# Kernel optimization log

Measured on AMD Instinct MI355X. Metric: run time of the kernel, lower is better.

## Reference

```python
import jax, jax.numpy as jnp
import numpy as np

SEQ, BATCH, EMBED = 2048, 4, 768
NUM_HEADS = 12
HEAD_DIM = EMBED // NUM_HEADS
SCALING = HEAD_DIM ** -0.5


def setup_inputs() -> dict:
    key = jax.random.key(0)
    ks = jax.random.split(key, 9)
    std = 0.02
    d = {"x": jax.random.normal(ks[0], (SEQ, BATCH, EMBED), dtype=jnp.float32)}
    for i, n in enumerate(["q", "k", "v", "out"]):
        d[f"W{n}"] = jax.random.normal(ks[1 + 2 * i], (EMBED, EMBED), dtype=jnp.float32) * std
        d[f"b{n}"] = jax.random.normal(ks[2 + 2 * i], (EMBED,), dtype=jnp.float32) * std
    return d


def reference(x, Wq, bq, Wk, bk, Wv, bv, Wout, bout):
    # x: [tgt_len, bsz, embed_dim] (fairseq seq-first layout per forward body)
    T, B, E = x.shape
    H, Dh = NUM_HEADS, HEAD_DIM

    q = (x @ Wq.T + bq) * SCALING          # [T, B, E]
    k = x @ Wk.T + bk
    v = x @ Wv.T + bv

    # view(T, B*H, Dh).transpose(0, 1) -> [B*H, T, Dh]
    q = q.reshape(T, B * H, Dh).transpose(1, 0, 2)
    k = k.reshape(T, B * H, Dh).transpose(1, 0, 2)
    v = v.reshape(T, B * H, Dh).transpose(1, 0, 2)

    # bmm: [B*H, T, T] attention scores (full O(T^2) matrix, as in the original)
    scores = jnp.einsum('bqd,bkd->bqk', q, k)
    # util_softmax with onnx_trace=True: softmax in float32, then cast back
    probs = jax.nn.softmax(scores.astype(jnp.float32), axis=-1).astype(scores.dtype)
    # dropout p=0.0 -> identity

    attn = jnp.einsum('bqk,bkd->bqd', probs, v)           # [B*H, T, Dh]
    attn = attn.transpose(1, 0, 2).reshape(T, B, E)       # [T, B, E]
    return attn @ Wout.T + bout
```

## Files before the change

kernel.cpp:

```cpp
#include <hip/hip_runtime.h>
#include <hip/hip_bf16.h>

#define SEQ 2048
#define BATCH 4
#define EMBED 768
#define NHEAD 12
#define HDIM 64
#define NROWS (SEQ*BATCH)
#define GH (BATCH*NHEAD)
#define KVBLK 64

typedef __bf16 bf16;
typedef __attribute__((ext_vector_type(4))) __bf16 bf16x4;
typedef __attribute__((ext_vector_type(8))) __bf16 bf16x8;
typedef __attribute__((ext_vector_type(4))) float f32x4;

#define LOG2E 1.44269504088896340736f

__global__ __launch_bounds__(256) void cvt_kernel(const float* __restrict__ in,
                                                  bf16* __restrict__ out, int n4) {
  int i = blockIdx.x * 256 + threadIdx.x;
  if (i >= n4) return;
  float4 v = reinterpret_cast<const float4*>(in)[i];
  bf16x4 o;
  o[0] = (bf16)v.x; o[1] = (bf16)v.y; o[2] = (bf16)v.z; o[3] = (bf16)v.w;
  reinterpret_cast<bf16x4*>(out)[i] = o;
}

__global__ __launch_bounds__(256) void cvt_w4(const float* __restrict__ Wq,
                                              const float* __restrict__ Wk,
                                              const float* __restrict__ Wv,
                                              const float* __restrict__ Wo,
                                              bf16* __restrict__ Wqkvb,
                                              bf16* __restrict__ Wob) {
  const int n4 = EMBED * EMBED / 4;
  int i = blockIdx.x * 256 + threadIdx.x;
  if (i >= n4) return;
  const float* src;
  bf16* dst;
  switch (blockIdx.y) {
    case 0: src = Wq; dst = Wqkvb; break;
    case 1: src = Wk; dst = Wqkvb + EMBED * EMBED; break;
    case 2: src = Wv; dst = Wqkvb + 2 * EMBED * EMBED; break;
    default: src = Wo; dst = Wob; break;
  }
  float4 v = reinterpret_cast<const float4*>(src)[i];
  bf16x4 o;
  o[0] = (bf16)v.x; o[1] = (bf16)v.y; o[2] = (bf16)v.z; o[3] = (bf16)v.w;
  reinterpret_cast<bf16x4*>(dst)[i] = o;
}

__global__ __launch_bounds__(256) void gemm_qkv(const bf16* __restrict__ A,
                                                const bf16* __restrict__ B,
                                                const float* __restrict__ bq,
                                                const float* __restrict__ bk,
                                                const float* __restrict__ bv,
                                                bf16* __restrict__ Qh,
                                                bf16* __restrict__ Kh,
                                                bf16* __restrict__ Vt) {
  constexpr int K = EMBED;
  __shared__ bf16 As[128 * 32];
  __shared__ bf16 Bs[128 * 32];
  const int tid = threadIdx.x;
  const int l = tid & 63;
  const int w = tid >> 6;
  const int row0 = blockIdx.x * 128;
  const int col0 = blockIdx.y * 128;
  const int wm = (w >> 1) * 64;
  const int wn = (w & 1) * 64;
  const int l15 = l & 15, l4 = l >> 4;

  f32x4 acc[4][4] = {};

  for (int k0 = 0; k0 < K; k0 += 32) {
#pragma unroll
    for (int i = 0; i < 2; ++i) {
      int c = tid + i * 256;
      int r = c >> 2, cc = c & 3;
      __builtin_amdgcn_global_load_lds(
          (const __attribute__((address_space(1))) void*)(A + (size_t)(row0 + r) * K + k0 + cc * 8),
          (__attribute__((address_space(3))) void*)(As + c * 8), 16, 0, 0);
    }
#pragma unroll
    for (int i = 0; i < 2; ++i) {
      int c = tid + i * 256;
      int r = c >> 2, cc = c & 3;
      __builtin_amdgcn_global_load_lds(
          (const __attribute__((address_space(1))) void*)(B + (size_t)(col0 + r) * K + k0 + cc * 8),
          (__attribute__((address_space(3))) void*)(Bs + c * 8), 16, 0, 0);
    }
    __syncthreads();

    bf16x8 af[4], bfr[4];
#pragma unroll
    for (int i = 0; i < 4; ++i)
      af[i] = *reinterpret_cast<const bf16x8*>(&As[(wm + i * 16 + l15) * 32 + l4 * 8]);
#pragma unroll
    for (int j = 0; j < 4; ++j)
      bfr[j] = *reinterpret_cast<const bf16x8*>(&Bs[(wn + j * 16 + l15) * 32 + l4 * 8]);
#pragma unroll
    for (int i = 0; i < 4; ++i)
#pragma unroll
      for (int j = 0; j < 4; ++j)
        acc[i][j] = __builtin_amdgcn_mfma_f32_16x16x32_bf16(af[i], bfr[j], acc[i][j], 0, 0, 0);
    __syncthreads();
  }

  const int sel = blockIdx.y / 6;
  const float* bias = sel == 0 ? bq : (sel == 1 ? bk : bv);
  const int colbase = col0 - sel * EMBED;
#pragma unroll
  for (int i = 0; i < 4; ++i) {
#pragma unroll
    for (int j = 0; j < 4; ++j) {
      int col = colbase + wn + j * 16 + l15;
      float bia = bias[col];
#pragma unroll
      for (int r = 0; r < 4; ++r) {
        int row = row0 + wm + i * 16 + l4 * 4 + r;
        float v = acc[i][j][r] + bia;
        int t = row >> 2, bb = row & 3;
        int hh = col >> 6, d = col & 63;
        int g = bb * NHEAD + hh;
        if (sel == 0)      Qh[((size_t)g * SEQ + t) * HDIM + d] = (bf16)(v * (0.125f * LOG2E));
        else if (sel == 1) Kh[((size_t)g * SEQ + t) * HDIM + d] = (bf16)v;
        else               Vt[((size_t)g * HDIM + d) * SEQ + t] = (bf16)v;
      }
    }
  }
}

__global__ __launch_bounds__(256) void gemm_out(const bf16* __restrict__ A,
                                                const bf16* __restrict__ B,
                                                const float* __restrict__ bias,
                                                float* __restrict__ outp) {
  constexpr int K = EMBED;
  __shared__ bf16 As[128 * 32];
  __shared__ bf16 Bs[128 * 32];
  const int tid = threadIdx.x;
  const int l = tid & 63;
  const int w = tid >> 6;
  const int row0 = blockIdx.x * 128;
  const int col0 = blockIdx.y * 128;
  const int wm = (w >> 1) * 64;
  const int wn = (w & 1) * 64;
  const int l15 = l & 15, l4 = l >> 4;

  f32x4 acc[4][4] = {};

  for (int k0 = 0; k0 < K; k0 += 32) {
#pragma unroll
    for (int i = 0; i < 2; ++i) {
      int c = tid + i * 256;
      int r = c >> 2, cc = c & 3;
      __builtin_amdgcn_global_load_lds(
          (const __attribute__((address_space(1))) void*)(A + (size_t)(row0 + r) * K + k0 + cc * 8),
          (__attribute__((address_space(3))) void*)(As + c * 8), 16, 0, 0);
    }
#pragma unroll
    for (int i = 0; i < 2; ++i) {
      int c = tid + i * 256;
      int r = c >> 2, cc = c & 3;
      __builtin_amdgcn_global_load_lds(
          (const __attribute__((address_space(1))) void*)(B + (size_t)(col0 + r) * K + k0 + cc * 8),
          (__attribute__((address_space(3))) void*)(Bs + c * 8), 16, 0, 0);
    }
    __syncthreads();

    bf16x8 af[4], bfr[4];
#pragma unroll
    for (int i = 0; i < 4; ++i)
      af[i] = *reinterpret_cast<const bf16x8*>(&As[(wm + i * 16 + l15) * 32 + l4 * 8]);
#pragma unroll
    for (int j = 0; j < 4; ++j)
      bfr[j] = *reinterpret_cast<const bf16x8*>(&Bs[(wn + j * 16 + l15) * 32 + l4 * 8]);
#pragma unroll
    for (int i = 0; i < 4; ++i)
#pragma unroll
      for (int j = 0; j < 4; ++j)
        acc[i][j] = __builtin_amdgcn_mfma_f32_16x16x32_bf16(af[i], bfr[j], acc[i][j], 0, 0, 0);
    __syncthreads();
  }

#pragma unroll
  for (int i = 0; i < 4; ++i) {
#pragma unroll
    for (int j = 0; j < 4; ++j) {
      int col = col0 + wn + j * 16 + l15;
      float bia = bias[col];
#pragma unroll
      for (int r = 0; r < 4; ++r) {
        int row = row0 + wm + i * 16 + l4 * 4 + r;
        outp[(size_t)row * EMBED + col] = acc[i][j][r] + bia;
      }
    }
  }
}

__global__ __launch_bounds__(256, 4) void attn_kernel(const bf16* __restrict__ Qh,
                                                      const bf16* __restrict__ Kh,
                                                      const bf16* __restrict__ Vt,
                                                      bf16* __restrict__ attnb) {
  const int g = blockIdx.x % GH;
  const int q0 = (blockIdx.x / GH) * 128;
  const int tid = threadIdx.x;
  const int w = tid >> 6, l = tid & 63;
  const int l15 = l & 15, l4 = l >> 4;
  const int qw = q0 + w * 32;

  __shared__ bf16 Ks[2][KVBLK * HDIM];
  __shared__ bf16 Vs[HDIM * KVBLK];
  __shared__ bf16 P_all[4][32 * 64];

  bf16* P = (bf16*)P_all[w];
  const bf16* Qp = Qh + (size_t)g * SEQ * HDIM;
  const bf16* Kp = Kh + (size_t)g * SEQ * HDIM;
  const bf16* Vp = Vt + (size_t)g * HDIM * SEQ;

#define STAGE_K(buf, kv0)                                                               \
  do {                                                                                  \
    _Pragma("unroll") for (int i = 0; i < 2; ++i) {                                     \
      int t = i * 256 + tid;                                                            \
      int r = t >> 3, c = t & 7;                                                        \
      __builtin_amdgcn_global_load_lds(                                                 \
          (const __attribute__((address_space(1))) void*)(Kp + (size_t)((kv0) + r) * HDIM + ((c ^ (r & 7)) * 8)), \
          (__attribute__((address_space(3))) void*)(&Ks[buf][t * 8]), 16, 0, 0);        \
    }                                                                                   \
  } while (0)

#define STAGE_V(kv0)                                                                    \
  do {                                                                                  \
    _Pragma("unroll") for (int i = 0; i < 2; ++i) {                                     \
      int t = i * 256 + tid;                                                            \
      int r = t >> 3, c = t & 7;                                                        \
      __builtin_amdgcn_global_load_lds(                                                 \
          (const __attribute__((address_space(1))) void*)(Vp + (size_t)r * SEQ + (kv0) + ((c ^ (r & 7)) * 8)), \
          (__attribute__((address_space(3))) void*)(&Vs[t * 8]), 16, 0, 0);             \
    }                                                                                   \
  } while (0)

  bf16x8 aq[2][2];
#pragma unroll
  for (int qf = 0; qf < 2; ++qf)
#pragma unroll
    for (int ks = 0; ks < 2; ++ks)
      aq[qf][ks] = *reinterpret_cast<const bf16x8*>(
          Qp + (size_t)(qw + qf * 16 + l15) * HDIM + ks * 32 + l4 * 8);

  bf16x8 vone;
#pragma unroll
  for (int i = 0; i < 8; ++i) vone[i] = (bf16)1.0f;

  f32x4 acco[2][4] = {};
  f32x4 accs[2] = {};

  STAGE_K(0, 0);
  __syncthreads();

  int cur = 0;
  for (int kv0 = 0; kv0 < SEQ; kv0 += KVBLK) {
    STAGE_V(kv0);
    STAGE_K(cur ^ 1, (kv0 + KVBLK) & (SEQ - 1));

    f32x4 s[2][4] = {};
#pragma unroll
    for (int kf = 0; kf < 4; ++kf) {
      int row = kf * 16 + l15;
#pragma unroll
      for (int ks = 0; ks < 2; ++ks) {
        bf16x8 bk = *reinterpret_cast<const bf16x8*>(
            &Ks[cur][row * 64 + (((ks * 4 + l4) ^ (row & 7)) * 8)]);
        __builtin_amdgcn_s_setprio(1);
        s[0][kf] = __builtin_amdgcn_mfma_f32_16x16x32_bf16(bk, aq[0][ks], s[0][kf], 0, 0, 0);
        s[1][kf] = __builtin_amdgcn_mfma_f32_16x16x32_bf16(bk, aq[1][ks], s[1][kf], 0, 0, 0);
        __builtin_amdgcn_s_setprio(0);
      }
    }

#pragma unroll
    for (int qf = 0; qf < 2; ++qf) {
      int prow = qf * 16 + l15;
#pragma unroll
      for (int kf = 0; kf < 4; ++kf) {
        float p0 = exp2f(s[qf][kf][0]);
        float p1 = exp2f(s[qf][kf][1]);
        float p2 = exp2f(s[qf][kf][2]);
        float p3 = exp2f(s[qf][kf][3]);
        bf16x4 pk;
        pk[0] = (bf16)p0; pk[1] = (bf16)p1; pk[2] = (bf16)p2; pk[3] = (bf16)p3;
        int chunk = (2 * kf + (l4 >> 1)) ^ (prow & 7);
        *reinterpret_cast<bf16x4*>(&P[prow * 64 + chunk * 8 + (l4 & 1) * 4]) = pk;
      }
    }

    asm volatile("s_waitcnt vmcnt(2)" ::: "memory");

#pragma unroll
    for (int ks = 0; ks < 2; ++ks) {
      bf16x8 ap[2];
#pragma unroll
      for (int qf = 0; qf < 2; ++qf) {
        int prow = qf * 16 + l15;
        int lc = ks * 4 + l4;
        ap[qf] = *reinterpret_cast<const bf16x8*>(P + prow * 64 + ((lc ^ (prow & 7)) << 3));
      }
#pragma unroll
      for (int df = 0; df < 4; ++df) {
        int row = df * 16 + l15;
        bf16x8 bv = *reinterpret_cast<const bf16x8*>(
            &Vs[row * 64 + (((ks * 4 + l4) ^ (row & 7)) * 8)]);
        __builtin_amdgcn_s_setprio(1);
        acco[0][df] = __builtin_amdgcn_mfma_f32_16x16x32_bf16(ap[0], bv, acco[0][df], 0, 0, 0);
        acco[1][df] = __builtin_amdgcn_mfma_f32_16x16x32_bf16(ap[1], bv, acco[1][df], 0, 0, 0);
        __builtin_amdgcn_s_setprio(0);
      }
      __builtin_amdgcn_s_setprio(1);
      accs[0] = __builtin_amdgcn_mfma_f32_16x16x32_bf16(ap[0], vone, accs[0], 0, 0, 0);
      accs[1] = __builtin_amdgcn_mfma_f32_16x16x32_bf16(ap[1], vone, accs[1], 0, 0, 0);
      __builtin_amdgcn_s_setprio(0);
    }
    __syncthreads();
    cur ^= 1;
  }

  const int bb = g / NHEAD, hh = g % NHEAD;
#pragma unroll
  for (int qf = 0; qf < 2; ++qf)
#pragma unroll
    for (int r = 0; r < 4; ++r) {
      float rinv = __builtin_amdgcn_rcpf(accs[qf][r]);
      int tq = qw + qf * 16 + l4 * 4 + r;
#pragma unroll
      for (int df = 0; df < 4; ++df) {
        int d = df * 16 + l15;
        attnb[((size_t)tq * BATCH + bb) * EMBED + hh * HDIM + d] = (bf16)(acco[qf][df][r] * rinv);
      }
    }
}

extern "C" void kernel_launch(void* const* d_in, const int* in_sizes, int n_in,
                              void* d_out, int out_size, void* d_ws, size_t ws_size,
                              hipStream_t stream) {
  const float* x  = (const float*)d_in[0];
  const float* Wq = (const float*)d_in[1];
  const float* bq = (const float*)d_in[2];
  const float* Wk = (const float*)d_in[3];
  const float* bk = (const float*)d_in[4];
  const float* Wv = (const float*)d_in[5];
  const float* bv = (const float*)d_in[6];
  const float* Wo = (const float*)d_in[7];
  const float* bo = (const float*)d_in[8];
  float* out = (float*)d_out;

  char* ws = (char*)d_ws;
  bf16* xb    = (bf16*)(ws + 0);
  bf16* Wqkvb = (bf16*)(ws + 12582912);
  bf16* Wob   = (bf16*)(ws + 16121856);
  bf16* Qh    = (bf16*)(ws + 17301504);
  bf16* Kh    = (bf16*)(ws + 29884416);
  bf16* Vt    = (bf16*)(ws + 42467328);
  bf16* attnb = (bf16*)(ws + 55050240);

  cvt_kernel<<<6144, 256, 0, stream>>>(x, xb, NROWS * EMBED / 4);
  cvt_w4<<<dim3(576, 4), 256, 0, stream>>>(Wq, Wk, Wv, Wo, Wqkvb, Wob);

  gemm_qkv<<<dim3(NROWS / 128, 18), 256, 0, stream>>>(xb, Wqkvb, bq, bk, bv, Qh, Kh, Vt);

  attn_kernel<<<GH * (SEQ / 128), 256, 0, stream>>>(Qh, Kh, Vt, attnb);

  gemm_out<<<dim3(NROWS / 128, EMBED / 128), 256, 0, stream>>>(attnb, Wob, bo, out);
}
```

Measured before the change: 168.3 us.

## Split attention KV range into two halves and combine partial outputs

Each attention workgroup now processes only half of the key/value sequence, doubling the grid from 768 to 1536 blocks to improve occupancy across compute units. Unnormalized partial outputs go to two bf16 buffers (reusing the xb workspace and attnb) along with per-row exp-sums. A new combine kernel adds the partials and normalizes. This works without rescaling because the kernel does not subtract a running max. It adds an extra pass over the attention output and rounds the unnormalized partials to bf16.

```diff
diff --git a/kernel.cpp b/kernel.cpp
--- a/kernel.cpp
+++ b/kernel.cpp
@@ -9,6 +9,7 @@
 #define NROWS (SEQ*BATCH)
 #define GH (BATCH*NHEAD)
 #define KVBLK 64
+#define KVHALF (SEQ/2)
 
 typedef __bf16 bf16;
 typedef __attribute__((ext_vector_type(4))) __bf16 bf16x4;
@@ -200,9 +201,14 @@
 __global__ __launch_bounds__(256, 4) void attn_kernel(const bf16* __restrict__ Qh,
                                                       const bf16* __restrict__ Kh,
                                                       const bf16* __restrict__ Vt,
-                                                      bf16* __restrict__ attnb) {
+                                                      bf16* __restrict__ O0,
+                                                      bf16* __restrict__ O1,
+                                                      float* __restrict__ Sums) {
   const int g = blockIdx.x % GH;
-  const int q0 = (blockIdx.x / GH) * 128;
+  const int r2 = blockIdx.x / GH;
+  const int half = r2 & 1;
+  const int q0 = (r2 >> 1) * 128;
+  const int kvbase = half * KVHALF;
   const int tid = threadIdx.x;
   const int w = tid >> 6, l = tid & 63;
   const int l15 = l & 15, l4 = l >> 4;
@@ -254,13 +260,13 @@
   f32x4 acco[2][4] = {};
   f32x4 accs[2] = {};
 
-  STAGE_K(0, 0);
+  STAGE_K(0, kvbase);
   __syncthreads();
 
   int cur = 0;
-  for (int kv0 = 0; kv0 < SEQ; kv0 += KVBLK) {
+  for (int kv0 = kvbase; kv0 < kvbase + KVHALF; kv0 += KVBLK) {
     STAGE_V(kv0);
-    STAGE_K(cur ^ 1, (kv0 + KVBLK) & (SEQ - 1));
+    STAGE_K(cur ^ 1, kvbase + (((kv0 - kvbase) + KVBLK) & (KVHALF - 1)));
 
     f32x4 s[2][4] = {};
 #pragma unroll
@@ -323,19 +329,43 @@
     cur ^= 1;
   }
 
+  bf16* Op = half ? O1 : O0;
+  float* Sp = Sums + (size_t)half * GH * SEQ + (size_t)g * SEQ;
   const int bb = g / NHEAD, hh = g % NHEAD;
 #pragma unroll
   for (int qf = 0; qf < 2; ++qf)
 #pragma unroll
     for (int r = 0; r < 4; ++r) {
-      float rinv = __builtin_amdgcn_rcpf(accs[qf][r]);
       int tq = qw + qf * 16 + l4 * 4 + r;
+      if (l15 == 0) Sp[tq] = accs[qf][r];
 #pragma unroll
       for (int df = 0; df < 4; ++df) {
         int d = df * 16 + l15;
-        attnb[((size_t)tq * BATCH + bb) * EMBED + hh * HDIM + d] = (bf16)(acco[qf][df][r] * rinv);
-      }
-    }
+        Op[((size_t)tq * BATCH + bb) * EMBED + hh * HDIM + d] = (bf16)acco[qf][df][r];
+      }
+    }
+}
+
+__global__ __launch_bounds__(256) void attn_combine(const bf16* __restrict__ O0,
+                                                    const bf16* __restrict__ O1,
+                                                    const float* __restrict__ Sums,
+                                                    bf16* __restrict__ attnb) {
+  int i = blockIdx.x * 256 + threadIdx.x;
+  int flat = i * 8;
+  int row = flat / EMBED;
+  int e = flat - row * EMBED;
+  int tq = row >> 2, bb = row & 3;
+  int hh = e >> 6;
+  int g = bb * NHEAD + hh;
+  float s = Sums[(size_t)g * SEQ + tq] + Sums[(size_t)GH * SEQ + (size_t)g * SEQ + tq];
+  float rinv = __builtin_amdgcn_rcpf(s);
+  bf16x8 a0 = *reinterpret_cast<const bf16x8*>(O0 + flat);
+  bf16x8 a1 = *reinterpret_cast<const bf16x8*>(O1 + flat);
+  bf16x8 o;
+#pragma unroll
+  for (int j = 0; j < 8; ++j)
+    o[j] = (bf16)(((float)a0[j] + (float)a1[j]) * rinv);
+  *reinterpret_cast<bf16x8*>(attnb + flat) = o;
 }
 
 extern "C" void kernel_launch(void* const* d_in, const int* in_sizes, int n_in,
@@ -360,13 +390,15 @@
   bf16* Kh    = (bf16*)(ws + 29884416);
   bf16* Vt    = (bf16*)(ws + 42467328);
   bf16* attnb = (bf16*)(ws + 55050240);
+  float* Sums = (float*)(ws + 67633152);
 
   cvt_kernel<<<6144, 256, 0, stream>>>(x, xb, NROWS * EMBED / 4);
   cvt_w4<<<dim3(576, 4), 256, 0, stream>>>(Wq, Wk, Wv, Wo, Wqkvb, Wob);
 
   gemm_qkv<<<dim3(NROWS / 128, 18), 256, 0, stream>>>(xb, Wqkvb, bq, bk, bv, Qh, Kh, Vt);
 
-  attn_kernel<<<GH * (SEQ / 128), 256, 0, stream>>>(Qh, Kh, Vt, attnb);
+  attn_kernel<<<GH * (SEQ / 128) * 2, 256, 0, stream>>>(Qh, Kh, Vt, xb, attnb, Sums);
+  attn_combine<<<NROWS * EMBED / 8 / 256, 256, 0, stream>>>(xb, attnb, Sums, attnb);
 
   gemm_out<<<dim3(NROWS / 128, EMBED / 128), 256, 0, stream>>>(attnb, Wob, bo, out);
 }
```

Measured after the change: 172.5 us. +2.5%, slower.
